# Performance work log

Hardware: AMD Instinct MI355X
Metric: run time of the kernel (lower is better)

## Reference

```python
import jax, jax.numpy as jnp
import numpy as np

NUM_HEADS = 12
NUM_LANDMARKS = 64
EPS_REG = 1e-4


def setup_inputs() -> dict:
    key = jax.random.key(0)
    k1, k2, k3 = jax.random.split(key, 3)
    B, N, C = 4, 4096, 768
    x = jax.random.normal(k1, (B, N, C), dtype=jnp.float32)
    w_qkv = jax.random.normal(k2, (3 * C, C), dtype=jnp.float32) * (C ** -0.5)
    w_proj = jax.random.normal(k3, (C, C), dtype=jnp.float32) * (C ** -0.5)
    b_proj = jnp.zeros((C,), dtype=jnp.float32)
    return {"x": x, "w_qkv": w_qkv, "w_proj": w_proj, "b_proj": b_proj}


def _landmark_pool(t, m):
    # t: [B, H, N, D]; assumes N % m == 0 (true for chosen shapes)
    B, H, N, D = t.shape
    seg = N // m
    return t.reshape(B, H, m, seg, D).mean(axis=3)


def reference(x, w_qkv, w_proj, b_proj):
    B, N, C = x.shape
    H = NUM_HEADS
    D = C // H
    m = min(NUM_LANDMARKS, N)
    scale = D ** -0.5

    qkv = x @ w_qkv.T                              # [B, N, 3C]
    qkv = qkv.reshape(B, N, 3, H, D).transpose(2, 0, 3, 1, 4)
    q, k, v = qkv[0], qkv[1], qkv[2]               # [B, H, N, D]

    q_lm = _landmark_pool(q, m)                    # [B, H, m, D]
    k_lm = _landmark_pool(k, m)                    # [B, H, m, D]

    attn_q_km = jax.nn.softmax(jnp.einsum('bhnd,bhmd->bhnm', q, k_lm) * scale, axis=-1)
    attn_qm_km = jax.nn.softmax(jnp.einsum('bhld,bhmd->bhlm', q_lm, k_lm) * scale, axis=-1)
    attn_qm_k = jax.nn.softmax(jnp.einsum('bhmd,bhnd->bhmn', q_lm, k) * scale, axis=-1)

    eye = jnp.eye(m, dtype=attn_qm_km.dtype)
    inv_mid = jnp.linalg.inv(attn_qm_km + EPS_REG * eye)   # [B, H, m, m]

    out = attn_q_km @ (inv_mid @ (attn_qm_k @ v))          # [B, H, N, D]
    out = out.transpose(0, 2, 1, 3).reshape(B, N, C)
    out = out @ w_proj.T + b_proj
    return out
```

## Files before the change

### kernel.cpp

```cpp
#include <hip/hip_runtime.h>

typedef unsigned short u16;
typedef __attribute__((ext_vector_type(8))) short bf16x8;
typedef __attribute__((ext_vector_type(8))) unsigned short u16x8;
typedef __attribute__((ext_vector_type(4))) unsigned short u16x4;
typedef __attribute__((ext_vector_type(4))) float f32x4;

#define NB 4
#define NH 12
#define NSEQ 4096
#define NC 768
#define ND 64
#define NM 64
#define NBH 48

__device__ __forceinline__ float b2f(u16 u){ unsigned v = ((unsigned)u)<<16; return __builtin_bit_cast(float, v); }
__device__ __forceinline__ u16 f2b(float f){ unsigned u = __builtin_bit_cast(unsigned, f); u = u + 0x7FFFu + ((u>>16)&1u); return (u16)(u>>16); }
__device__ __forceinline__ void split2(float f, u16& h, u16& l){
  h = f2b(f);
  l = f2b(f - b2f(h));
}

typedef const __attribute__((address_space(1))) unsigned int guint;
typedef __attribute__((address_space(3))) unsigned int luint;
__device__ __forceinline__ void gload16(const void* g, void* l){
  __builtin_amdgcn_global_load_lds((guint*)g, (luint*)l, 16, 0, 0);
}

__device__ __forceinline__ f32x4 mfma16x16(bf16x8 a, bf16x8 b, f32x4 c){
  return __builtin_amdgcn_mfma_f32_16x16x32_bf16(a, b, c, 0, 0, 0);
}

__global__ __launch_bounds__(256) void k_split(const float* __restrict__ src, u16* __restrict__ dh,
                                               u16* __restrict__ dl, int n4){
  int i = blockIdx.x*256 + threadIdx.x;
  if (i >= n4) return;
  f32x4 v = ((const f32x4*)src)[i];
  u16x4 hh, ll;
  #pragma unroll
  for (int e=0;e<4;++e){ u16 hb, lb; split2(v[e], hb, lb); hh[e]=hb; ll[e]=lb; }
  ((u16x4*)dh)[i] = hh; ((u16x4*)dl)[i] = ll;
}


__global__ __launch_bounds__(256) void k_qkv(const u16* __restrict__ xh, const u16* __restrict__ xl,
                                             const u16* __restrict__ wh, const u16* __restrict__ wl,
                                             u16* __restrict__ qh, u16* __restrict__ ql,
                                             u16* __restrict__ kh, u16* __restrict__ kl,
                                             u16* __restrict__ vTh, u16* __restrict__ vTl){
  __shared__ u16 Ah[8192], Al[8192], Bh[8192], Bl[8192];
  const int K = NC;
  int tid = threadIdx.x, wave = tid>>6, lane = tid&63;
  int wm = wave>>1, wn = wave&1;
  int m0 = blockIdx.y*128, n0 = blockIdx.x*128;
  int srow = lane>>3;
  int scol = ((lane&7) ^ srow)*8;
  const u16* src0; u16* dst0;
  if (wave==0){ src0 = xh + (size_t)m0*K; dst0 = Ah; }
  else if (wave==1){ src0 = xl + (size_t)m0*K; dst0 = Al; }
  else if (wave==2){ src0 = wh + (size_t)n0*K; dst0 = Bh; }
  else            { src0 = wl + (size_t)n0*K; dst0 = Bl; }
  f32x4 acc[4][4] = {};
  for (int k0=0; k0<K; k0+=64){
    #pragma unroll
    for (int it=0; it<16; ++it){
      int r = it*8;
      gload16(&src0[(size_t)(r+srow)*K + k0 + scol], &dst0[r*64]);
    }
    __syncthreads();
    #pragma unroll
    for (int kk=0; kk<2; ++kk){
      int sl = ((kk*4 + (lane>>4)) ^ (lane&7))*8;
      bf16x8 a_h[4], a_l[4], b_h[4], b_l[4];
      #pragma unroll
      for (int i=0;i<4;++i){
        int ro = (wm*64+i*16+(lane&15))*64 + sl;
        a_h[i] = *(const bf16x8*)&Ah[ro]; a_l[i] = *(const bf16x8*)&Al[ro];
      }
      #pragma unroll
      for (int j=0;j<4;++j){
        int ro = (wn*64+j*16+(lane&15))*64 + sl;
        b_h[j] = *(const bf16x8*)&Bh[ro]; b_l[j] = *(const bf16x8*)&Bl[ro];
      }
      #pragma unroll
      for (int i=0;i<4;++i)
        #pragma unroll
        for (int j=0;j<4;++j){
          acc[i][j] = mfma16x16(a_h[i], b_h[j], acc[i][j]);
          acc[i][j] = mfma16x16(a_h[i], b_l[j], acc[i][j]);
          acc[i][j] = mfma16x16(a_l[i], b_h[j], acc[i][j]);
        }
    }
    __syncthreads();
  }
  int rb = (lane>>4)*4, cb = lane&15;
  #pragma unroll
  for (int j=0;j<4;++j){
    int gn = n0 + wn*64 + j*16 + cb;
    int s = gn/768; int rem = gn - s*768; int hd = rem>>6, d = rem&63;
    u16* dh = (s==0)? qh : (s==1)? kh : vTh;
    u16* dl = (s==0)? ql : (s==1)? kl : vTl;
    #pragma unroll
    for (int i=0;i<4;++i){
      #pragma unroll
      for (int r=0;r<4;++r){
        int gm = m0 + wm*64 + i*16 + rb + r;
        int b_ = gm>>12, n = gm & 4095;
        size_t idx;
        if (s==2) idx = (((size_t)(b_*NH + hd))*ND + d)*NSEQ + n;
        else      idx = (((size_t)(b_*NH + hd))*NSEQ + n)*ND + d;
        u16 hb, lb; split2(acc[i][j][r], hb, lb);
        dh[idx] = hb; dl[idx] = lb;
      }
    }
  }
}

__global__ __launch_bounds__(256) void k_proj(const u16* __restrict__ Hh, const u16* __restrict__ Hl,
                                              const u16* __restrict__ wh, const u16* __restrict__ wl,
                                              const float* __restrict__ bias, float* __restrict__ out){
  __shared__ u16 Ah[8192], Al[8192], Bh[8192], Bl[8192];
  const int K = NC;
  int tid = threadIdx.x, wave = tid>>6, lane = tid&63;
  int wm = wave>>1, wn = wave&1;
  int m0 = blockIdx.y*128, n0 = blockIdx.x*128;
  int srow = lane>>3;
  int scol = ((lane&7) ^ srow)*8;
  const u16* src0; u16* dst0;
  if (wave==0){ src0 = Hh + (size_t)m0*K; dst0 = Ah; }
  else if (wave==1){ src0 = Hl + (size_t)m0*K; dst0 = Al; }
  else if (wave==2){ src0 = wh + (size_t)n0*K; dst0 = Bh; }
  else            { src0 = wl + (size_t)n0*K; dst0 = Bl; }
  f32x4 acc[4][4] = {};
  for (int k0=0; k0<K; k0+=64){
    #pragma unroll
    for (int it=0; it<16; ++it){
      int r = it*8;
      gload16(&src0[(size_t)(r+srow)*K + k0 + scol], &dst0[r*64]);
    }
    __syncthreads();
    #pragma unroll
    for (int kk=0; kk<2; ++kk){
      int sl = ((kk*4 + (lane>>4)) ^ (lane&7))*8;
      bf16x8 a_h[4], a_l[4], b_h[4], b_l[4];
      #pragma unroll
      for (int i=0;i<4;++i){
        int ro = (wm*64+i*16+(lane&15))*64 + sl;
        a_h[i] = *(const bf16x8*)&Ah[ro]; a_l[i] = *(const bf16x8*)&Al[ro];
      }
      #pragma unroll
      for (int j=0;j<4;++j){
        int ro = (wn*64+j*16+(lane&15))*64 + sl;
        b_h[j] = *(const bf16x8*)&Bh[ro]; b_l[j] = *(const bf16x8*)&Bl[ro];
      }
      #pragma unroll
      for (int i=0;i<4;++i)
        #pragma unroll
        for (int j=0;j<4;++j){
          acc[i][j] = mfma16x16(a_h[i], b_h[j], acc[i][j]);
          acc[i][j] = mfma16x16(a_h[i], b_l[j], acc[i][j]);
          acc[i][j] = mfma16x16(a_l[i], b_h[j], acc[i][j]);
        }
    }
    __syncthreads();
  }
  int rb = (lane>>4)*4, cb = lane&15;
  #pragma unroll
  for (int j=0;j<4;++j){
    int gn = n0 + wn*64 + j*16 + cb;
    float bb = bias[gn];
    #pragma unroll
    for (int i=0;i<4;++i){
      #pragma unroll
      for (int r=0;r<4;++r){
        int gm = m0 + wm*64 + i*16 + rb + r;
        out[(size_t)gm*NC + gn] = acc[i][j][r] + bb;
      }
    }
  }
}

__global__ __launch_bounds__(64) void k_pool(const u16* __restrict__ qh, const u16* __restrict__ ql,
                                             const u16* __restrict__ kh, const u16* __restrict__ kl,
                                             float* __restrict__ qlmf, float* __restrict__ klmf,
                                             u16* __restrict__ qlmh, u16* __restrict__ qlml,
                                             u16* __restrict__ klmh, u16* __restrict__ klml){
  int l = blockIdx.x, bh = blockIdx.y, d = threadIdx.x;
  size_t base = ((size_t)bh*NSEQ + l*64)*ND + d;
  float sq = 0.f, sk = 0.f;
  #pragma unroll 8
  for (int j=0;j<64;++j){
    size_t o = base + (size_t)j*ND;
    sq += b2f(qh[o]) + b2f(ql[o]);
    sk += b2f(kh[o]) + b2f(kl[o]);
  }
  sq *= (1.f/64.f); sk *= (1.f/64.f);
  size_t o = ((size_t)bh*NM + l)*ND + d;
  qlmf[o] = sq; klmf[o] = sk;
  u16 hb, lb;
  split2(sq, hb, lb); qlmh[o] = hb; qlml[o] = lb;
  split2(sk, hb, lb); klmh[o] = hb; klml[o] = lb;
}

__global__ __launch_bounds__(256) void k_s2(const u16* __restrict__ qlmh, const u16* __restrict__ qlml,
                                            const u16* __restrict__ kh, const u16* __restrict__ kl,
                                            float* __restrict__ s2f){
  int chunk = blockIdx.x, bh = blockIdx.y;
  int tid = threadIdx.x, wave = tid>>6, lane = tid&63;
  const u16* Ahp = qlmh + (size_t)bh*NM*ND;
  const u16* Alp = qlml + (size_t)bh*NM*ND;
  const u16* Bhp = kh + (size_t)bh*NSEQ*ND;
  const u16* Blp = kl + (size_t)bh*NSEQ*ND;
  int nbase = chunk*256 + wave*64;
  f32x4 acc[4][4] = {};
  #pragma unroll
  for (int kk=0; kk<2; ++kk){
    int koff = kk*32 + (lane>>4)*8;
    bf16x8 a_h[4], a_l[4], b_h[4], b_l[4];
    #pragma unroll
    for (int i=0;i<4;++i){
      size_t ro = (size_t)(i*16+(lane&15))*ND + koff;
      a_h[i] = *(const bf16x8*)&Ahp[ro]; a_l[i] = *(const bf16x8*)&Alp[ro];
    }
    #pragma unroll
    for (int j=0;j<4;++j){
      size_t ro = (size_t)(nbase + j*16 + (lane&15))*ND + koff;
      b_h[j] = *(const bf16x8*)&Bhp[ro]; b_l[j] = *(const bf16x8*)&Blp[ro];
    }
    #pragma unroll
    for (int i=0;i<4;++i)
      #pragma unroll
      for (int j=0;j<4;++j){
        acc[i][j] = mfma16x16(a_h[i], b_h[j], acc[i][j]);
        acc[i][j] = mfma16x16(a_h[i], b_l[j], acc[i][j]);
        acc[i][j] = mfma16x16(a_l[i], b_h[j], acc[i][j]);
      }
  }
  int rb = (lane>>4)*4, cb = lane&15;
  #pragma unroll
  for (int i=0;i<4;++i)
    #pragma unroll
    for (int j=0;j<4;++j)
      #pragma unroll
      for (int r=0;r<4;++r){
        int l = i*16 + rb + r; int n = nbase + j*16 + cb;
        s2f[((size_t)bh*NM + l)*NSEQ + n] = acc[i][j][r]*0.125f;
      }
}

__global__ __launch_bounds__(256) void k_sm(float* __restrict__ s2region){
  int row = blockIdx.x;
  int tid = threadIdx.x, lane = tid&63, wid = tid>>6;
  __shared__ float redm[4], reds[4];
  const float* src = s2region + (size_t)row*NSEQ;
  const f32x4* ps = (const f32x4*)(src + (size_t)tid*16);
  f32x4 v0 = ps[0], v1 = ps[1], v2 = ps[2], v3 = ps[3];
  float vals[16];
  #pragma unroll
  for (int e=0;e<4;++e){ vals[e]=v0[e]; vals[4+e]=v1[e]; vals[8+e]=v2[e]; vals[12+e]=v3[e]; }
  float mx = -1e30f;
  #pragma unroll
  for (int j=0;j<16;++j) mx = fmaxf(mx, vals[j]);
  for (int off=32; off; off>>=1) mx = fmaxf(mx, __shfl_xor(mx, off));
  if (lane==0) redm[wid] = mx;
  __syncthreads();
  mx = fmaxf(fmaxf(redm[0],redm[1]), fmaxf(redm[2],redm[3]));
  float s = 0.f;
  #pragma unroll
  for (int j=0;j<16;++j){ vals[j] = __expf(vals[j]-mx); s += vals[j]; }
  for (int off=32; off; off>>=1) s += __shfl_xor(s, off);
  if (lane==0) reds[wid] = s;
  __syncthreads();
  s = reds[0]+reds[1]+reds[2]+reds[3];
  float inv = 1.f/s;
  u16* rh = (u16*)s2region + (size_t)row*8192;
  u16* rl = rh + 4096;
  u16x8 oh0, oh1, ol0, ol1;
  #pragma unroll
  for (int j=0;j<8;++j){
    u16 hb, lb;
    split2(vals[j]*inv, hb, lb);   oh0[j]=hb; ol0[j]=lb;
    split2(vals[8+j]*inv, hb, lb); oh1[j]=hb; ol1[j]=lb;
  }
  ((u16x8*)(rh + (size_t)tid*16))[0] = oh0;
  ((u16x8*)(rh + (size_t)tid*16))[1] = oh1;
  ((u16x8*)(rl + (size_t)tid*16))[0] = ol0;
  ((u16x8*)(rl + (size_t)tid*16))[1] = ol1;
}

__global__ __launch_bounds__(256) void k_t1(const u16* __restrict__ p2base, const u16* __restrict__ vTh,
                                            const u16* __restrict__ vTl, float* __restrict__ t1p){
  int kb = blockIdx.x, bh = blockIdx.y;
  int tid = threadIdx.x, wave = tid>>6, lane = tid&63;
  int arow = wave*16 + (lane&15);
  const u16* rowp = p2base + (size_t)(bh*64 + arow)*8192;
  const u16* Bh = vTh + (size_t)bh*ND*NSEQ;
  const u16* Bl = vTl + (size_t)bh*ND*NSEQ;
  f32x4 acc[4] = {};
  for (int ks=0; ks<16; ++ks){
    int koff = kb*512 + ks*32 + (lane>>4)*8;
    bf16x8 a_h = *(const bf16x8*)&rowp[koff];
    bf16x8 a_l = *(const bf16x8*)&rowp[4096 + koff];
    #pragma unroll
    for (int j=0;j<4;++j){
      size_t ro = (size_t)(j*16+(lane&15))*NSEQ + koff;
      bf16x8 b_h = *(const bf16x8*)&Bh[ro];
      bf16x8 b_l = *(const bf16x8*)&Bl[ro];
      acc[j] = mfma16x16(a_h, b_h, acc[j]);
      acc[j] = mfma16x16(a_h, b_l, acc[j]);
      acc[j] = mfma16x16(a_l, b_h, acc[j]);
    }
  }
  int rb = (lane>>4)*4, cb = lane&15;
  #pragma unroll
  for (int j=0;j<4;++j)
    #pragma unroll
    for (int r=0;r<4;++r){
      int l = wave*16 + rb + r; int d = j*16 + cb;
      t1p[((size_t)(kb*NBH + bh)*NM + l)*ND + d] = acc[j][r];
    }
}

__global__ __launch_bounds__(256) void k_mid(const float* __restrict__ qlmf, const float* __restrict__ klmf,
                                            const float* __restrict__ t1p,
                                            u16* __restrict__ w2th, u16* __restrict__ w2tl){
  __shared__ float M[64*68];
  __shared__ float T[64*68];
  __shared__ int piv_s;
  int bh = blockIdx.x, tid = threadIdx.x;
  int r = tid>>2, qd = tid&3;
  const float* qrow  = qlmf + (size_t)bh*NM*ND + r*64;
  const float* kbase = klmf + (size_t)bh*NM*ND;
  float qv[64];
  #pragma unroll
  for (int e=0;e<16;++e){
    f32x4 t4 = ((const f32x4*)qrow)[e];
    qv[e*4]=t4[0]; qv[e*4+1]=t4[1]; qv[e*4+2]=t4[2]; qv[e*4+3]=t4[3];
  }
  float sv[16];
  #pragma unroll
  for (int mi=0;mi<16;++mi){
    const float* krow = kbase + (size_t)(qd*16+mi)*64;
    float a = 0.f;
    #pragma unroll
    for (int e=0;e<16;++e){
      f32x4 k4 = ((const f32x4*)krow)[e];
      a += qv[e*4]*k4[0] + qv[e*4+1]*k4[1] + qv[e*4+2]*k4[2] + qv[e*4+3]*k4[3];
    }
    sv[mi] = a*0.125f;
  }
  float mx = sv[0];
  #pragma unroll
  for (int mi=1;mi<16;++mi) mx = fmaxf(mx, sv[mi]);
  mx = fmaxf(mx, __shfl_xor(mx,1)); mx = fmaxf(mx, __shfl_xor(mx,2));
  float sum = 0.f;
  #pragma unroll
  for (int mi=0;mi<16;++mi){ sv[mi] = __expf(sv[mi]-mx); sum += sv[mi]; }
  sum += __shfl_xor(sum,1); sum += __shfl_xor(sum,2);
  float sinv = 1.f/sum;
  #pragma unroll
  for (int mi=0;mi<16;++mi){
    int m = qd*16+mi;
    float p = sv[mi]*sinv;
    if (m == r) p += 1e-4f;
    M[r*68+m] = p;
  }
  #pragma unroll
  for (int q=0;q<4;++q){
    int c = qd*16 + q*4;
    f32x4 a = {};
    #pragma unroll
    for (int kb=0;kb<8;++kb)
      a += *(const f32x4*)&t1p[((size_t)(kb*NBH + bh)*NM + r)*ND + c];
    *(f32x4*)&T[r*68+c] = a;
  }
  __syncthreads();
  for (int kp=0; kp<64; ++kp){
    if (tid < 64){
      float val = (tid >= kp) ? fabsf(M[tid*68+kp]) : -1.f;
      int idx = tid;
      #pragma unroll
      for (int off=32; off; off>>=1){
        float ov = __shfl_xor(val, off); int oi = __shfl_xor(idx, off);
        if (ov > val || (ov == val && oi < idx)){ val = ov; idx = oi; }
      }
      if (tid == 0) piv_s = idx;
    }
    __syncthreads();
    int p = piv_s;
    if (r == kp){
      float pinv = 1.f / M[p*68+kp];
      f32x4 mk[4], mp[4], tk[4], tp_[4];
      #pragma unroll
      for (int q=0;q<4;++q){
        int c = qd*16 + q*4;
        mk[q] = *(const f32x4*)&M[kp*68+c]; mp[q] = *(const f32x4*)&M[p*68+c];
        tk[q] = *(const f32x4*)&T[kp*68+c]; tp_[q] = *(const f32x4*)&T[p*68+c];
      }
      #pragma unroll
      for (int q=0;q<4;++q){
        int c = qd*16 + q*4;
        *(f32x4*)&M[p*68+c] = mk[q];       *(f32x4*)&T[p*68+c] = tk[q];
        *(f32x4*)&M[kp*68+c] = mp[q]*pinv; *(f32x4*)&T[kp*68+c] = tp_[q]*pinv;
      }
    }
    __syncthreads();
    if (r != kp){
      float f = M[r*68+kp];
      #pragma unroll
      for (int q=0;q<4;++q){
        int c = qd*16 + q*4;
        f32x4 pm = *(const f32x4*)&M[kp*68+c];
        f32x4 om = *(const f32x4*)&M[r*68+c];
        *(f32x4*)&M[r*68+c] = om - f*pm;
        f32x4 pt = *(const f32x4*)&T[kp*68+c];
        f32x4 ot = *(const f32x4*)&T[r*68+c];
        *(f32x4*)&T[r*68+c] = ot - f*pt;
      }
    }
    __syncthreads();
  }
  int d = tid>>2, qs = tid&3;
  #pragma unroll
  for (int li=0; li<16; ++li){
    int l = qs*16 + li;
    float xv = T[l*68 + d];
    u16 hb, lb; split2(xv, hb, lb);
    size_t o = ((size_t)bh*ND + d)*NM + l;
    w2th[o] = hb; w2tl[o] = lb;
  }
}

__global__ __launch_bounds__(256) void k_final(const u16* __restrict__ qh, const u16* __restrict__ ql,
                                               const u16* __restrict__ klmh, const u16* __restrict__ klml,
                                               const u16* __restrict__ w2th, const u16* __restrict__ w2tl,
                                               u16* __restrict__ Hh, u16* __restrict__ Hl){
  __shared__ u16 Ph[4*4096], Pl[4*4096];
  int chunk = blockIdx.x, bh = blockIdx.y;
  int b_ = bh/NH, hd = bh - b_*NH;
  int tid = threadIdx.x, wave = tid>>6, lane = tid&63;
  int n0 = chunk*256 + wave*64;
  const u16* qhp = qh + ((size_t)bh*NSEQ + n0)*ND;
  const u16* qlp = ql + ((size_t)bh*NSEQ + n0)*ND;
  const u16* Kh = klmh + (size_t)bh*NM*ND;
  const u16* Kl = klml + (size_t)bh*NM*ND;
  const u16* Wh = w2th + (size_t)bh*ND*NM;
  const u16* Wl = w2tl + (size_t)bh*ND*NM;
  u16* Phw = Ph + wave*4096;
  u16* Plw = Pl + wave*4096;
  f32x4 accs[4][4] = {};
  #pragma unroll
  for (int kk=0; kk<2; ++kk){
    int koff = kk*32 + (lane>>4)*8;
    bf16x8 a_h[4], a_l[4], b_h[4], b_l[4];
    #pragma unroll
    for (int i=0;i<4;++i){
      size_t ro = (size_t)(i*16+(lane&15))*ND + koff;
      a_h[i] = *(const bf16x8*)&qhp[ro]; a_l[i] = *(const bf16x8*)&qlp[ro];
    }
    #pragma unroll
    for (int j=0;j<4;++j){
      size_t ro = (size_t)(j*16+(lane&15))*ND + koff;
      b_h[j] = *(const bf16x8*)&Kh[ro]; b_l[j] = *(const bf16x8*)&Kl[ro];
    }
    #pragma unroll
    for (int i=0;i<4;++i)
      #pragma unroll
      for (int j=0;j<4;++j){
        accs[i][j] = mfma16x16(a_h[i], b_h[j], accs[i][j]);
        accs[i][j] = mfma16x16(a_h[i], b_l[j], accs[i][j]);
        accs[i][j] = mfma16x16(a_l[i], b_h[j], accs[i][j]);
      }
  }
  #pragma unroll
  for (int i=0;i<4;++i)
    #pragma unroll
    for (int j=0;j<4;++j) accs[i][j] *= 0.125f;
  int rb = (lane>>4)*4, cb = lane&15;
  #pragma unroll
  for (int i=0;i<4;++i){
    #pragma unroll
    for (int r=0;r<4;++r){
      float mx = -1e30f;
      #pragma unroll
      for (int j=0;j<4;++j) mx = fmaxf(mx, accs[i][j][r]);
      #pragma unroll
      for (int off=1; off<16; off<<=1) mx = fmaxf(mx, __shfl_xor(mx, off));
      float e[4]; float sum = 0.f;
      #pragma unroll
      for (int j=0;j<4;++j){ e[j] = __expf(accs[i][j][r]-mx); sum += e[j]; }
      #pragma unroll
      for (int off=1; off<16; off<<=1) sum += __shfl_xor(sum, off);
      float inv = 1.f/sum;
      int row = i*16 + rb + r;
      #pragma unroll
      for (int j=0;j<4;++j){
        u16 hb, lb; split2(e[j]*inv, hb, lb);
        int col = j*16 + cb;
        int scol = (((col>>3) ^ (row&7))<<3) | (col&7);
        Phw[row*64 + scol] = hb;
        Plw[row*64 + scol] = lb;
      }
    }
  }
  __syncthreads();
  f32x4 acco[4][4] = {};
  #pragma unroll
  for (int kk=0; kk<2; ++kk){
    int koff = kk*32 + (lane>>4)*8;
    int sl = ((kk*4 + (lane>>4)) ^ (lane&7))*8;
    bf16x8 a_h[4], a_l[4], b_h[4], b_l[4];
    #pragma unroll
    for (int i=0;i<4;++i){
      int ro = (i*16+(lane&15))*64 + sl;
      a_h[i] = *(const bf16x8*)&Phw[ro]; a_l[i] = *(const bf16x8*)&Plw[ro];
    }
    #pragma unroll
    for (int j=0;j<4;++j){
      size_t ro = (size_t)(j*16+(lane&15))*64 + koff;
      b_h[j] = *(const bf16x8*)&Wh[ro]; b_l[j] = *(const bf16x8*)&Wl[ro];
    }
    #pragma unroll
    for (int i=0;i<4;++i)
      #pragma unroll
      for (int j=0;j<4;++j){
        acco[i][j] = mfma16x16(a_h[i], b_h[j], acco[i][j]);
        acco[i][j] = mfma16x16(a_h[i], b_l[j], acco[i][j]);
        acco[i][j] = mfma16x16(a_l[i], b_h[j], acco[i][j]);
      }
  }
  #pragma unroll
  for (int i=0;i<4;++i)
    #pragma unroll
    for (int j=0;j<4;++j)
      #pragma unroll
      for (int r=0;r<4;++r){
        int n = n0 + i*16 + rb + r;
        int d = j*16 + cb;
        size_t o = ((size_t)(b_*NSEQ + n))*NC + hd*64 + d;
        u16 hb, lb; split2(acco[i][j][r], hb, lb);
        Hh[o] = hb; Hl[o] = lb;
      }
}

__global__ void k_sent(float* out){ out[0] = 1.0e9f; }

#define OFF_QH     0ull
#define OFF_QL     25165824ull
#define OFF_KH     50331648ull
#define OFF_KL     75497472ull
#define OFF_VTH    100663296ull
#define OFF_VTL    125829120ull
#define OFF_S2     150994944ull
#define OFF_QLMF   201326592ull
#define OFF_KLMF   202113024ull
#define OFF_QLMH   202899456ull
#define OFF_QLML   203292672ull
#define OFF_KLMH   203685888ull
#define OFF_KLML   204079104ull
#define OFF_W2TH   204472320ull
#define OFF_W2TL   204865536ull
#define OFF_T1P    205258752ull
#define OFF_WQH    211550208ull
#define OFF_WQL    215089152ull
#define OFF_WPH    218628096ull
#define OFF_WPL    219807744ull
#define WS_NEEDED  220987392ull

extern "C" void kernel_launch(void* const* d_in, const int* in_sizes, int n_in,
                              void* d_out, int out_size, void* d_ws, size_t ws_size,
                              hipStream_t stream){
  const float* x     = (const float*)d_in[0];
  const float* wqkv  = (const float*)d_in[1];
  const float* wproj = (const float*)d_in[2];
  const float* bproj = (const float*)d_in[3];
  float* out = (float*)d_out;
  char* ws = (char*)d_ws;
  if (ws_size < WS_NEEDED){ k_sent<<<1,1,0,stream>>>(out); return; }
  u16* qh = (u16*)(ws + OFF_QH);  u16* ql = (u16*)(ws + OFF_QL);
  u16* kh = (u16*)(ws + OFF_KH);  u16* kl = (u16*)(ws + OFF_KL);
  u16* vTh = (u16*)(ws + OFF_VTH); u16* vTl = (u16*)(ws + OFF_VTL);
  u16* xh = (u16*)(ws + OFF_S2);
  u16* xl = (u16*)(ws + OFF_S2 + 25165824ull);
  float* s2f = (float*)(ws + OFF_S2);
  u16* p2base = (u16*)(ws + OFF_S2);
  u16* Hh = (u16*)(ws + OFF_S2);
  u16* Hl = (u16*)(ws + OFF_S2 + 25165824ull);
  float* qlmf = (float*)(ws + OFF_QLMF);
  float* klmf = (float*)(ws + OFF_KLMF);
  u16* qlmh = (u16*)(ws + OFF_QLMH); u16* qlml = (u16*)(ws + OFF_QLML);
  u16* klmh = (u16*)(ws + OFF_KLMH); u16* klml = (u16*)(ws + OFF_KLML);
  u16* w2th = (u16*)(ws + OFF_W2TH); u16* w2tl = (u16*)(ws + OFF_W2TL);
  float* t1p = (float*)(ws + OFF_T1P);
  u16* wqh = (u16*)(ws + OFF_WQH); u16* wql = (u16*)(ws + OFF_WQL);
  u16* wph = (u16*)(ws + OFF_WPH); u16* wpl = (u16*)(ws + OFF_WPL);

  k_split    <<<12288, 256, 0, stream>>>(x, xh, xl, 3145728);
  k_split    <<<1728,  256, 0, stream>>>(wqkv, wqh, wql, 442368);
  k_split    <<<576,   256, 0, stream>>>(wproj, wph, wpl, 147456);
  k_qkv      <<<dim3(18,128), 256, 0, stream>>>(xh, xl, wqh, wql, qh, ql, kh, kl, vTh, vTl);
  k_pool     <<<dim3(64,48),   64, 0, stream>>>(qh, ql, kh, kl, qlmf, klmf, qlmh, qlml, klmh, klml);
  k_s2       <<<dim3(16,48),  256, 0, stream>>>(qlmh, qlml, kh, kl, s2f);
  k_sm       <<<3072,         256, 0, stream>>>(s2f);
  k_t1       <<<dim3(8,48),   256, 0, stream>>>(p2base, vTh, vTl, t1p);
  k_mid      <<<48,           256, 0, stream>>>(qlmf, klmf, t1p, w2th, w2tl);
  k_final    <<<dim3(16,48),  256, 0, stream>>>(qh, ql, klmh, klml, w2th, w2tl, Hh, Hl);
  k_proj     <<<dim3(6,128),  256, 0, stream>>>(Hh, Hl, wph, wpl, bproj, out);
}
```

Measured before the change: 580.4 us.

## Fuse landmark pooling into QKV GEMM epilogue and coalesce V transpose via LDS

Landmark means for q and k are now computed in the QKV GEMM epilogue with cross-lane shuffles, and the separate k_pool kernel is removed. That kernel re-read the full q/k hi/lo arrays. The V-transpose output is staged through LDS so the vT stores become contiguous 16-byte writes instead of scattered 2-byte stores. The cost is extra epilogue work and LDS syncs. Means are now taken from fp32 accumulators rather than the rounded hi+lo pairs, so results may differ very slightly.

```diff
diff --git a/kernel.cpp b/kernel.cpp
--- a/kernel.cpp
+++ b/kernel.cpp
@@ -42,13 +42,15 @@
   ((u16x4*)dh)[i] = hh; ((u16x4*)dl)[i] = ll;
 }
 
-
 __global__ __launch_bounds__(256) void k_qkv(const u16* __restrict__ xh, const u16* __restrict__ xl,
                                              const u16* __restrict__ wh, const u16* __restrict__ wl,
                                              u16* __restrict__ qh, u16* __restrict__ ql,
                                              u16* __restrict__ kh, u16* __restrict__ kl,
-                                             u16* __restrict__ vTh, u16* __restrict__ vTl){
-  __shared__ u16 Ah[8192], Al[8192], Bh[8192], Bl[8192];
+                                             u16* __restrict__ vTh, u16* __restrict__ vTl,
+                                             float* __restrict__ qlmf, float* __restrict__ klmf,
+                                             u16* __restrict__ qlmh, u16* __restrict__ qlml,
+                                             u16* __restrict__ klmh, u16* __restrict__ klml){
+  __shared__ u16 lds[32768];
   const int K = NC;
   int tid = threadIdx.x, wave = tid>>6, lane = tid&63;
   int wm = wave>>1, wn = wave&1;
@@ -56,10 +58,10 @@
   int srow = lane>>3;
   int scol = ((lane&7) ^ srow)*8;
   const u16* src0; u16* dst0;
-  if (wave==0){ src0 = xh + (size_t)m0*K; dst0 = Ah; }
-  else if (wave==1){ src0 = xl + (size_t)m0*K; dst0 = Al; }
-  else if (wave==2){ src0 = wh + (size_t)n0*K; dst0 = Bh; }
-  else            { src0 = wl + (size_t)n0*K; dst0 = Bl; }
+  if (wave==0){ src0 = xh + (size_t)m0*K; dst0 = lds; }
+  else if (wave==1){ src0 = xl + (size_t)m0*K; dst0 = lds+8192; }
+  else if (wave==2){ src0 = wh + (size_t)n0*K; dst0 = lds+16384; }
+  else            { src0 = wl + (size_t)n0*K; dst0 = lds+24576; }
   f32x4 acc[4][4] = {};
   for (int k0=0; k0<K; k0+=64){
     #pragma unroll
@@ -75,12 +77,12 @@
       #pragma unroll
       for (int i=0;i<4;++i){
         int ro = (wm*64+i*16+(lane&15))*64 + sl;
-        a_h[i] = *(const bf16x8*)&Ah[ro]; a_l[i] = *(const bf16x8*)&Al[ro];
+        a_h[i] = *(const bf16x8*)&lds[ro]; a_l[i] = *(const bf16x8*)&lds[8192+ro];
       }
       #pragma unroll
       for (int j=0;j<4;++j){
         int ro = (wn*64+j*16+(lane&15))*64 + sl;
-        b_h[j] = *(const bf16x8*)&Bh[ro]; b_l[j] = *(const bf16x8*)&Bl[ro];
+        b_h[j] = *(const bf16x8*)&lds[16384+ro]; b_l[j] = *(const bf16x8*)&lds[24576+ro];
       }
       #pragma unroll
       for (int i=0;i<4;++i)
@@ -94,24 +96,69 @@
     __syncthreads();
   }
   int rb = (lane>>4)*4, cb = lane&15;
-  #pragma unroll
-  for (int j=0;j<4;++j){
-    int gn = n0 + wn*64 + j*16 + cb;
-    int s = gn/768; int rem = gn - s*768; int hd = rem>>6, d = rem&63;
-    u16* dh = (s==0)? qh : (s==1)? kh : vTh;
-    u16* dl = (s==0)? ql : (s==1)? kl : vTl;
-    #pragma unroll
-    for (int i=0;i<4;++i){
-      #pragma unroll
-      for (int r=0;r<4;++r){
-        int gm = m0 + wm*64 + i*16 + rb + r;
-        int b_ = gm>>12, n = gm & 4095;
-        size_t idx;
-        if (s==2) idx = (((size_t)(b_*NH + hd))*ND + d)*NSEQ + n;
-        else      idx = (((size_t)(b_*NH + hd))*NSEQ + n)*ND + d;
-        u16 hb, lb; split2(acc[i][j][r], hb, lb);
-        dh[idx] = hb; dl[idx] = lb;
-      }
+  int b_ = m0>>12, nlo = m0&4095;
+  if (n0 < 1536){
+    int s = n0/768;
+    u16* dh = s ? kh : qh;
+    u16* dl = s ? kl : ql;
+    float* lmf = s ? klmf : qlmf;
+    u16* lmh = s ? klmh : qlmh;
+    u16* lml = s ? klml : qlml;
+    #pragma unroll
+    for (int j=0;j<4;++j){
+      int gn = n0 + wn*64 + j*16 + cb;
+      int rem = gn - s*768; int hd = rem>>6, d = rem&63;
+      #pragma unroll
+      for (int i=0;i<4;++i)
+        #pragma unroll
+        for (int r=0;r<4;++r){
+          int n = nlo + wm*64 + i*16 + rb + r;
+          size_t idx = (((size_t)(b_*NH + hd))*NSEQ + n)*ND + d;
+          u16 hb, lb; split2(acc[i][j][r], hb, lb);
+          dh[idx] = hb; dl[idx] = lb;
+        }
+      float tot = 0.f;
+      #pragma unroll
+      for (int i=0;i<4;++i)
+        #pragma unroll
+        for (int r=0;r<4;++r) tot += acc[i][j][r];
+      tot += __shfl_xor(tot, 16);
+      tot += __shfl_xor(tot, 32);
+      if (lane < 16){
+        int lseg = (nlo>>6) + wm;
+        float mean = tot * (1.f/64.f);
+        size_t o = (((size_t)(b_*NH + hd))*NM + lseg)*ND + d;
+        lmf[o] = mean;
+        u16 hb, lb; split2(mean, hb, lb);
+        lmh[o] = hb; lml[o] = lb;
+      }
+    }
+  } else {
+    const int TS = 136;
+    #pragma unroll
+    for (int part=0; part<2; ++part){
+      __syncthreads();
+      #pragma unroll
+      for (int j=0;j<4;++j){
+        int dcol = wn*64 + j*16 + cb;
+        #pragma unroll
+        for (int i=0;i<4;++i)
+          #pragma unroll
+          for (int r=0;r<4;++r){
+            int nrow = wm*64 + i*16 + rb + r;
+            u16 hb, lb; split2(acc[i][j][r], hb, lb);
+            lds[dcol*TS + nrow] = part ? lb : hb;
+          }
+      }
+      __syncthreads();
+      int drow = tid>>1, half = (tid&1)*64;
+      int remd = (n0 - 1536) + drow;
+      int hd = remd>>6, dd = remd&63;
+      u16* dst = (part ? vTl : vTh) + (((size_t)(b_*NH + hd))*ND + dd)*NSEQ + nlo + half;
+      const u16* srcl = &lds[drow*TS + half];
+      #pragma unroll
+      for (int e=0;e<8;++e)
+        *(u16x8*)(dst + e*8) = *(const u16x8*)(srcl + e*8);
     }
   }
 }
@@ -119,7 +166,7 @@
 __global__ __launch_bounds__(256) void k_proj(const u16* __restrict__ Hh, const u16* __restrict__ Hl,
                                               const u16* __restrict__ wh, const u16* __restrict__ wl,
                                               const float* __restrict__ bias, float* __restrict__ out){
-  __shared__ u16 Ah[8192], Al[8192], Bh[8192], Bl[8192];
+  __shared__ u16 lds[32768];
   const int K = NC;
   int tid = threadIdx.x, wave = tid>>6, lane = tid&63;
   int wm = wave>>1, wn = wave&1;
@@ -127,10 +174,10 @@
   int srow = lane>>3;
   int scol = ((lane&7) ^ srow)*8;
   const u16* src0; u16* dst0;
-  if (wave==0){ src0 = Hh + (size_t)m0*K; dst0 = Ah; }
-  else if (wave==1){ src0 = Hl + (size_t)m0*K; dst0 = Al; }
-  else if (wave==2){ src0 = wh + (size_t)n0*K; dst0 = Bh; }
-  else            { src0 = wl + (size_t)n0*K; dst0 = Bl; }
+  if (wave==0){ src0 = Hh + (size_t)m0*K; dst0 = lds; }
+  else if (wave==1){ src0 = Hl + (size_t)m0*K; dst0 = lds+8192; }
+  else if (wave==2){ src0 = wh + (size_t)n0*K; dst0 = lds+16384; }
+  else            { src0 = wl + (size_t)n0*K; dst0 = lds+24576; }
   f32x4 acc[4][4] = {};
   for (int k0=0; k0<K; k0+=64){
     #pragma unroll
@@ -146,12 +193,12 @@
       #pragma unroll
       for (int i=0;i<4;++i){
         int ro = (wm*64+i*16+(lane&15))*64 + sl;
-        a_h[i] = *(const bf16x8*)&Ah[ro]; a_l[i] = *(const bf16x8*)&Al[ro];
+        a_h[i] = *(const bf16x8*)&lds[ro]; a_l[i] = *(const bf16x8*)&lds[8192+ro];
       }
       #pragma unroll
       for (int j=0;j<4;++j){
         int ro = (wn*64+j*16+(lane&15))*64 + sl;
-        b_h[j] = *(const bf16x8*)&Bh[ro]; b_l[j] = *(const bf16x8*)&Bl[ro];
+        b_h[j] = *(const bf16x8*)&lds[16384+ro]; b_l[j] = *(const bf16x8*)&lds[24576+ro];
       }
       #pragma unroll
       for (int i=0;i<4;++i)
@@ -178,28 +225,6 @@
       }
     }
   }
-}
-
-__global__ __launch_bounds__(64) void k_pool(const u16* __restrict__ qh, const u16* __restrict__ ql,
-                                             const u16* __restrict__ kh, const u16* __restrict__ kl,
-                                             float* __restrict__ qlmf, float* __restrict__ klmf,
-                                             u16* __restrict__ qlmh, u16* __restrict__ qlml,
-                                             u16* __restrict__ klmh, u16* __restrict__ klml){
-  int l = blockIdx.x, bh = blockIdx.y, d = threadIdx.x;
-  size_t base = ((size_t)bh*NSEQ + l*64)*ND + d;
-  float sq = 0.f, sk = 0.f;
-  #pragma unroll 8
-  for (int j=0;j<64;++j){
-    size_t o = base + (size_t)j*ND;
-    sq += b2f(qh[o]) + b2f(ql[o]);
-    sk += b2f(kh[o]) + b2f(kl[o]);
-  }
-  sq *= (1.f/64.f); sk *= (1.f/64.f);
-  size_t o = ((size_t)bh*NM + l)*ND + d;
-  qlmf[o] = sq; klmf[o] = sk;
-  u16 hb, lb;
-  split2(sq, hb, lb); qlmh[o] = hb; qlml[o] = lb;
-  split2(sk, hb, lb); klmh[o] = hb; klml[o] = lb;
 }
 
 __global__ __launch_bounds__(256) void k_s2(const u16* __restrict__ qlmh, const u16* __restrict__ qlml,
@@ -598,8 +623,8 @@
   k_split    <<<12288, 256, 0, stream>>>(x, xh, xl, 3145728);
   k_split    <<<1728,  256, 0, stream>>>(wqkv, wqh, wql, 442368);
   k_split    <<<576,   256, 0, stream>>>(wproj, wph, wpl, 147456);
-  k_qkv      <<<dim3(18,128), 256, 0, stream>>>(xh, xl, wqh, wql, qh, ql, kh, kl, vTh, vTl);
-  k_pool     <<<dim3(64,48),   64, 0, stream>>>(qh, ql, kh, kl, qlmf, klmf, qlmh, qlml, klmh, klml);
+  k_qkv      <<<dim3(18,128), 256, 0, stream>>>(xh, xl, wqh, wql, qh, ql, kh, kl, vTh, vTl,
+                                                qlmf, klmf, qlmh, qlml, klmh, klml);
   k_s2       <<<dim3(16,48),  256, 0, stream>>>(qlmh, qlml, kh, kl, s2f);
   k_sm       <<<3072,         256, 0, stream>>>(s2f);
   k_t1       <<<dim3(8,48),   256, 0, stream>>>(p2base, vTh, vTl, t1p);
```

Result: faster. 515.7 us (-11.1%).
